# Optimization experiments

Measured on AMD Instinct MI355X. Metric: run time of the kernel, lower is better.

The kernel has to match this reference:

```python
import jax, jax.numpy as jnp
import numpy as np
import math

D_INNER = 512
D_STATE = 16
DT_RANK = 32
B_SZ = 2
L_SEQ = 4096


def setup_inputs() -> dict:
    key = jax.random.key(0)
    ks = jax.random.split(key, 6)
    x = jax.random.normal(ks[0], (B_SZ, L_SEQ, D_INNER), dtype=jnp.float32)
    # parameters (match torch init semantics closely enough for a numeric baseline)
    A = jnp.arange(1, D_STATE + 1, dtype=jnp.float32)
    A_log = jnp.broadcast_to(jnp.log(A)[None, :], (D_INNER, D_STATE)).copy()
    D_param = jnp.ones((D_INNER,), dtype=jnp.float32)
    # x_proj: Linear(d_inner -> dt_rank + 2*d_state), no bias
    W_xproj = jax.random.normal(ks[1], (DT_RANK + 2 * D_STATE, D_INNER), dtype=jnp.float32) / np.sqrt(D_INNER)
    # dt_proj: Linear(dt_rank -> d_inner) with special bias init
    W_dt = jax.random.normal(ks[2], (D_INNER, DT_RANK), dtype=jnp.float32) / np.sqrt(DT_RANK)
    dt_init = jnp.exp(jax.random.uniform(ks[3], (D_INNER,)) * (math.log(0.1) - math.log(0.001)) + math.log(0.001))
    b_dt = jnp.log(jnp.exp(dt_init) - 1.0)
    alpha = jnp.asarray(0.6, dtype=jnp.float32)
    beta_logit = jnp.asarray(math.log(0.99 / (1.0 - 0.99 + 1e-08)), dtype=jnp.float32)
    return {"x": x, "A_log": A_log, "D_param": D_param, "W_xproj": W_xproj,
            "W_dt": W_dt, "b_dt": b_dt, "alpha": alpha, "beta_logit": beta_logit}


def _momentum_ssm(x, A_log, D_param, W_xproj, W_dt, b_dt, alpha, beta_logit):
    # x: (B, L, D)
    proj = jnp.einsum('bld,pd->blp', x, W_xproj)            # (B, L, r+2N)
    dt_in = proj[..., :DT_RANK]
    Bp = proj[..., DT_RANK:DT_RANK + D_STATE]                # (B, L, N)
    Cp = proj[..., DT_RANK + D_STATE:]                       # (B, L, N)
    dt = jax.nn.softplus(jnp.einsum('blr,dr->bld', dt_in, W_dt) + b_dt)  # (B, L, D)
    A = -jnp.exp(A_log)                                      # (D, N)
    A_bar = jnp.exp(dt[..., None] * A[None, None])           # (B, L, D, N)
    # fused B_bar * x_t: dt * Bp * x
    inp = dt[..., None] * Bp[:, :, None, :] * x[..., None]   # (B, L, D, N)
    beta = jax.nn.sigmoid(beta_logit)

    # scan over time; carry (h, v): (B, D, N)
    h0 = jnp.zeros((x.shape[0], D_INNER, D_STATE), dtype=x.dtype)
    v0 = jnp.zeros_like(h0)

    def step(carry, ts):
        h, v = carry
        a_t, inp_t, c_t = ts                                 # (B,D,N), (B,D,N), (B,N)
        v = beta * v + alpha * inp_t
        h = a_t * h + v
        y = jnp.einsum('bdn,bn->bd', h, c_t)
        return (h, v), y

    xs = (jnp.moveaxis(A_bar, 1, 0), jnp.moveaxis(inp, 1, 0), jnp.moveaxis(Cp, 1, 0))
    _, ys = jax.lax.scan(step, (h0, v0), xs)                 # ys: (L, B, D)
    y = jnp.moveaxis(ys, 0, 1)                               # (B, L, D)
    return y + D_param * x


def reference(x, A_log, D_param, W_xproj, W_dt, b_dt, alpha, beta_logit):
    return _momentum_ssm(x, A_log, D_param, W_xproj, W_dt, b_dt, alpha, beta_logit)
```

## Files before the change

kernel.cpp:

```cpp
#include <hip/hip_runtime.h>


#define D_IN 512
#define D_ST 16
#define DTR  32
#define BSZ  2
#define LSEQ 4096
#define PDIM 64
#define NCH  128
#define LCH  (LSEQ / NCH)
#define LOG2E 1.44269504f

typedef __attribute__((ext_vector_type(8))) short short8;
typedef __attribute__((ext_vector_type(4))) float f32x4;

__device__ inline unsigned short bf16_rne(float f) {
  unsigned b = __float_as_uint(f);
  return (unsigned short)((b + 0x7fffu + ((b >> 16) & 1u)) >> 16);
}

__device__ inline void cvt8(const float4 u, const float4 v, short8& hi, short8& lo) {
  float f[8] = {u.x, u.y, u.z, u.w, v.x, v.y, v.z, v.w};
#pragma unroll
  for (int i = 0; i < 8; ++i) {
    unsigned short h = bf16_rne(f[i]);
    hi[i] = (short)h;
    float r = f[i] - __uint_as_float((unsigned)h << 16);
    lo[i] = (short)bf16_rne(r);
  }
}

__global__ __launch_bounds__(256) void k_wprep(const float* __restrict__ W,
                                               short* __restrict__ Whi,
                                               short* __restrict__ Wlo) {
  const int i = (blockIdx.x * 256 + threadIdx.x) * 4;
  float4 w = *(const float4*)(W + i);
  float f[4] = {w.x, w.y, w.z, w.w};
  unsigned short h[4], lo[4];
#pragma unroll
  for (int j = 0; j < 4; ++j) {
    h[j] = bf16_rne(f[j]);
    float r = f[j] - __uint_as_float((unsigned)h[j] << 16);
    lo[j] = bf16_rne(r);
  }
  *(uint2*)(Whi + i) = make_uint2(h[0] | ((unsigned)h[1] << 16), h[2] | ((unsigned)h[3] << 16));
  *(uint2*)(Wlo + i) = make_uint2(lo[0] | ((unsigned)lo[1] << 16), lo[2] | ((unsigned)lo[3] << 16));
}

#define MM3(ACC, AH, AL, BH, BL)                                        \
  ACC = __builtin_amdgcn_mfma_f32_16x16x32_bf16(AL, BH, ACC, 0, 0, 0);  \
  ACC = __builtin_amdgcn_mfma_f32_16x16x32_bf16(AH, BL, ACC, 0, 0, 0);  \
  ACC = __builtin_amdgcn_mfma_f32_16x16x32_bf16(AH, BH, ACC, 0, 0, 0);

#define LOADB(P, S)                                   \
  {                                                   \
    const int kb = ((S) & 15) * 32;                   \
    P##h0 = *(const short8*)(bh + kb);                \
    P##h1 = *(const short8*)(bh + 8192 + kb);         \
    P##h2 = *(const short8*)(bh + 16384 + kb);        \
    P##h3 = *(const short8*)(bh + 24576 + kb);        \
    P##l0 = *(const short8*)(bl + kb);                \
    P##l1 = *(const short8*)(bl + 8192 + kb);         \
    P##l2 = *(const short8*)(bl + 16384 + kb);        \
    P##l3 = *(const short8*)(bl + 24576 + kb);        \
  }

#define LOADA(Aa, Ab, S)                              \
  {                                                   \
    const int ka = ((S) & 15) * 32;                   \
    Aa = *(const float4*)(xr + ka);                   \
    Ab = *(const float4*)(xr + ka + 4);               \
  }

#define SUBSTEP(Aa, Ab, P, SA, SB)                    \
  {                                                   \
    short8 ahi, alo;                                  \
    cvt8(Aa, Ab, ahi, alo);                           \
    MM3(acc0, ahi, alo, P##h0, P##l0);                \
    MM3(acc1, ahi, alo, P##h1, P##l1);                \
    MM3(acc2, ahi, alo, P##h2, P##l2);                \
    MM3(acc3, ahi, alo, P##h3, P##l3);                \
    LOADB(P, SB);                                     \
    LOADA(Aa, Ab, SA);                                \
  }

__global__ __launch_bounds__(64) void k_proj(const float* __restrict__ x,
                                             const short* __restrict__ Whi,
                                             const short* __restrict__ Wlo,
                                             float* __restrict__ proj) {
  const int row0 = blockIdx.x * 16;
  const int l = threadIdx.x;
  const int m = l & 15;
  const int ko = (l >> 4) * 8;
  const float* xr = x + (size_t)(row0 + m) * D_IN + ko;
  const short* bh = Whi + (size_t)m * D_IN + ko;
  const short* bl = Wlo + (size_t)m * D_IN + ko;

  f32x4 acc0 = {0.f, 0.f, 0.f, 0.f}, acc1 = acc0, acc2 = acc0, acc3 = acc0;
  float4 A0a, A0b, A1a, A1b, A2a, A2b, A3a, A3b;
  short8 Xh0, Xh1, Xh2, Xh3, Xl0, Xl1, Xl2, Xl3;
  short8 Yh0, Yh1, Yh2, Yh3, Yl0, Yl1, Yl2, Yl3;
  LOADA(A0a, A0b, 0); LOADA(A1a, A1b, 1); LOADA(A2a, A2b, 2); LOADA(A3a, A3b, 3);
  LOADB(X, 0); LOADB(Y, 1);

#pragma unroll
  for (int it = 0; it < 4; ++it) {
    const int s = it * 4;
    SUBSTEP(A0a, A0b, X, s + 4, s + 2);
    SUBSTEP(A1a, A1b, Y, s + 5, s + 3);
    SUBSTEP(A2a, A2b, X, s + 6, s + 4);
    SUBSTEP(A3a, A3b, Y, s + 7, s + 5);
  }

  const int col = l & 15;
  const int r0 = (l >> 4) * 4;
#pragma unroll
  for (int r = 0; r < 4; ++r) {
    float* pr = proj + (size_t)(row0 + r0 + r) * PDIM + col;
    pr[0] = acc0[r]; pr[16] = acc1[r]; pr[32] = acc2[r]; pr[48] = acc3[r];
  }
}

__global__ __launch_bounds__(256) void k_dt(const float* __restrict__ proj,
                                            const float* __restrict__ W_dt,
                                            const float* __restrict__ b_dt,
                                            float* __restrict__ dt) {
  const int r0 = blockIdx.x * 8;
  const int d = blockIdx.y * 256 + threadIdx.x;
  float w[DTR];
  const float4* wp = (const float4*)(W_dt + (size_t)d * DTR);
#pragma unroll
  for (int i = 0; i < 8; ++i) ((float4*)w)[i] = wp[i];
  const float bb = b_dt[d];
#pragma unroll
  for (int r = 0; r < 8; ++r) {
    const float* pr = proj + (size_t)(r0 + r) * PDIM;
    float a0 = bb, a1 = 0.f, a2 = 0.f, a3 = 0.f;
#pragma unroll
    for (int k = 0; k < DTR; k += 4) {
      a0 = fmaf(pr[k + 0], w[k + 0], a0);
      a1 = fmaf(pr[k + 1], w[k + 1], a1);
      a2 = fmaf(pr[k + 2], w[k + 2], a2);
      a3 = fmaf(pr[k + 3], w[k + 3], a3);
    }
    float acc = (a0 + a1) + (a2 + a3);
    float sp = (acc > 20.f) ? acc : log1pf(__expf(acc));
    dt[(size_t)(r0 + r) * D_IN + d] = sp;
  }
}

#define S1_STEP(DC, XC, BC)                     \
  {                                             \
    sd += DC;                                   \
    bpow *= beta;                               \
    const float u = alpha * DC * XC;            \
    const float* Bf = (const float*)BC;         \
    _Pragma("unroll")                           \
    for (int n = 0; n < 16; ++n) {              \
      float a = exp2f(DC * A2[n]);              \
      v[n] = fmaf(beta, v[n], u * Bf[n]);       \
      h[n] = fmaf(a, h[n], v[n]);               \
      cv[n] = fmaf(a, cv[n], bpow);             \
    }                                           \
  }

__global__ __launch_bounds__(256) void k_scan1(const float* __restrict__ dt,
                                               const float* __restrict__ x,
                                               const float* __restrict__ proj,
                                               const float* __restrict__ A_log,
                                               const float* __restrict__ alpha_p,
                                               const float* __restrict__ beta_p,
                                               float* __restrict__ hh,
                                               float* __restrict__ vh,
                                               float* __restrict__ cvv,
                                               float* __restrict__ sdt) {
  const int c = blockIdx.x, b = blockIdx.z;
  const int d = blockIdx.y * 256 + threadIdx.x;
  const float alpha = alpha_p[0];
  const float beta = 1.f / (1.f + __expf(-beta_p[0]));
  float A2[D_ST];
  {
    const float4* ap = (const float4*)(A_log + (size_t)d * D_ST);
#pragma unroll
    for (int i = 0; i < 4; ++i) {
      float4 a4 = ap[i];
      A2[4 * i + 0] = -__expf(a4.x) * LOG2E;
      A2[4 * i + 1] = -__expf(a4.y) * LOG2E;
      A2[4 * i + 2] = -__expf(a4.z) * LOG2E;
      A2[4 * i + 3] = -__expf(a4.w) * LOG2E;
    }
  }
  float h[16] = {}, v[16] = {}, cv[16] = {};
  float bpow = 1.f, sd = 0.f;

  const int t0 = c * LCH;
  const float* dtp = dt + (size_t)b * LSEQ * D_IN + d;
  const float* xp = x + (size_t)b * LSEQ * D_IN + d;
  const float* bcp = proj + (size_t)b * LSEQ * PDIM + DTR;

  float d0 = dtp[(size_t)t0 * D_IN], x0v = xp[(size_t)t0 * D_IN];
  float d1 = dtp[(size_t)(t0 + 1) * D_IN], x1v = xp[(size_t)(t0 + 1) * D_IN];
  float4 B0[4], B1[4];
#pragma unroll
  for (int i = 0; i < 4; ++i) {
    B0[i] = *(const float4*)(bcp + (size_t)t0 * PDIM + 4 * i);
    B1[i] = *(const float4*)(bcp + (size_t)(t0 + 1) * PDIM + 4 * i);
  }

  for (int j = 0; j < LCH; j += 2) {
    const size_t ta = t0 + ((j + 2) & (LCH - 1));
    S1_STEP(d0, x0v, B0);
    d0 = dtp[ta * D_IN]; x0v = xp[ta * D_IN];
#pragma unroll
    for (int i = 0; i < 4; ++i) B0[i] = *(const float4*)(bcp + ta * PDIM + 4 * i);

    const size_t tb = t0 + ((j + 3) & (LCH - 1));
    S1_STEP(d1, x1v, B1);
    d1 = dtp[tb * D_IN]; x1v = xp[tb * D_IN];
#pragma unroll
    for (int i = 0; i < 4; ++i) B1[i] = *(const float4*)(bcp + tb * PDIM + 4 * i);
  }

  const size_t base = ((size_t)(b * NCH + c) * D_IN + d) * D_ST;
#pragma unroll
  for (int i = 0; i < 4; ++i) {
    *(float4*)(hh + base + 4 * i) = ((float4*)h)[i];
    *(float4*)(vh + base + 4 * i) = ((float4*)v)[i];
    *(float4*)(cvv + base + 4 * i) = ((float4*)cv)[i];
  }
  sdt[(size_t)(b * NCH + c) * D_IN + d] = sd;
}

__global__ __launch_bounds__(64) void k_fix(float* __restrict__ hh,
                                            float* __restrict__ vh,
                                            const float* __restrict__ cvv,
                                            const float* __restrict__ sdt,
                                            const float* __restrict__ A_log,
                                            const float* __restrict__ beta_p) {
  const int g = blockIdx.x * 64 + threadIdx.x;
  const int b = g >> 13;
  const int dn = g & 8191;
  const float beta = 1.f / (1.f + __expf(-beta_p[0]));
  const float A2 = -__expf(A_log[dn]) * LOG2E;
  float bL = beta;
#pragma unroll
  for (int i = 0; i < 5; ++i) bL *= bL;

  const size_t cs = (size_t)D_IN * D_ST;
  const size_t base = (size_t)b * NCH * cs + dn;
  const size_t sbase = (size_t)b * NCH * D_IN + (dn >> 4);

  float hg[4], vg[4], cg[4], sg[4];
#pragma unroll
  for (int i = 0; i < 4; ++i) {
    hg[i] = hh[base + i * cs];
    vg[i] = vh[base + i * cs];
    cg[i] = cvv[base + i * cs];
    sg[i] = sdt[sbase + i * D_IN];
  }
  float H = 0.f, V = 0.f;
  for (int c0 = 0; c0 < NCH; c0 += 4) {
    const int cp = (c0 + 4) & (NCH - 1);
    float hn[4], vn[4], cn[4], sn[4];
#pragma unroll
    for (int i = 0; i < 4; ++i) {
      hn[i] = hh[base + (size_t)(cp + i) * cs];
      vn[i] = vh[base + (size_t)(cp + i) * cs];
      cn[i] = cvv[base + (size_t)(cp + i) * cs];
      sn[i] = sdt[sbase + (size_t)(cp + i) * D_IN];
    }
#pragma unroll
    for (int i = 0; i < 4; ++i) {
      hh[base + (size_t)(c0 + i) * cs] = H;
      vh[base + (size_t)(c0 + i) * cs] = V;
      const float Pa = exp2f(sg[i] * A2);
      const float Hn = fmaf(Pa, H, fmaf(cg[i], V, hg[i]));
      V = fmaf(bL, V, vg[i]);
      H = Hn;
    }
#pragma unroll
    for (int i = 0; i < 4; ++i) { hg[i] = hn[i]; vg[i] = vn[i]; cg[i] = cn[i]; sg[i] = sn[i]; }
  }
}

#define S2_STEP(DC, XC, BC, TT)                                   \
  {                                                               \
    const float u = alpha * DC * XC;                              \
    const float* Bf = (const float*)BC;                           \
    float y0 = 0.f, y1 = 0.f, y2 = 0.f, y3 = 0.f;                 \
    _Pragma("unroll")                                             \
    for (int n = 0; n < 16; ++n) {                                \
      float a = exp2f(DC * A2[n]);                                \
      v[n] = fmaf(beta, v[n], u * Bf[n]);                         \
      h[n] = fmaf(a, h[n], v[n]);                                 \
      float hc = h[n] * Bf[16 + n];                               \
      if ((n & 3) == 0) y0 += hc;                                 \
      else if ((n & 3) == 1) y1 += hc;                            \
      else if ((n & 3) == 2) y2 += hc;                            \
      else y3 += hc;                                              \
    }                                                             \
    op[(size_t)(TT) * D_IN] = (y0 + y1) + (y2 + y3) + Dv * XC;    \
  }

__global__ __launch_bounds__(256) void k_scan2(const float* __restrict__ dt,
                                               const float* __restrict__ x,
                                               const float* __restrict__ proj,
                                               const float* __restrict__ A_log,
                                               const float* __restrict__ D_param,
                                               const float* __restrict__ alpha_p,
                                               const float* __restrict__ beta_p,
                                               const float* __restrict__ hh,
                                               const float* __restrict__ vh,
                                               float* __restrict__ out) {
  const int c = blockIdx.x, b = blockIdx.z;
  const int d = blockIdx.y * 256 + threadIdx.x;
  const float alpha = alpha_p[0];
  const float beta = 1.f / (1.f + __expf(-beta_p[0]));
  const float Dv = D_param[d];
  float A2[D_ST];
  {
    const float4* ap = (const float4*)(A_log + (size_t)d * D_ST);
#pragma unroll
    for (int i = 0; i < 4; ++i) {
      float4 a4 = ap[i];
      A2[4 * i + 0] = -__expf(a4.x) * LOG2E;
      A2[4 * i + 1] = -__expf(a4.y) * LOG2E;
      A2[4 * i + 2] = -__expf(a4.z) * LOG2E;
      A2[4 * i + 3] = -__expf(a4.w) * LOG2E;
    }
  }
  const size_t ibase = ((size_t)(b * NCH + c) * D_IN + d) * D_ST;
  float h[16], v[16];
#pragma unroll
  for (int i = 0; i < 4; ++i) {
    ((float4*)h)[i] = *(const float4*)(hh + ibase + 4 * i);
    ((float4*)v)[i] = *(const float4*)(vh + ibase + 4 * i);
  }

  const int t0 = c * LCH;
  const float* dtp = dt + (size_t)b * LSEQ * D_IN + d;
  const float* xp = x + (size_t)b * LSEQ * D_IN + d;
  const float* bcp = proj + (size_t)b * LSEQ * PDIM + DTR;
  float* op = out + (size_t)b * LSEQ * D_IN + d;

  float d0 = dtp[(size_t)t0 * D_IN], x0v = xp[(size_t)t0 * D_IN];
  float d1 = dtp[(size_t)(t0 + 1) * D_IN], x1v = xp[(size_t)(t0 + 1) * D_IN];
  float4 BC0[8], BC1[8];
#pragma unroll
  for (int i = 0; i < 8; ++i) {
    BC0[i] = *(const float4*)(bcp + (size_t)t0 * PDIM + 4 * i);
    BC1[i] = *(const float4*)(bcp + (size_t)(t0 + 1) * PDIM + 4 * i);
  }

  for (int j = 0; j < LCH; j += 2) {
    const size_t ta = t0 + ((j + 2) & (LCH - 1));
    S2_STEP(d0, x0v, BC0, t0 + j);
    d0 = dtp[ta * D_IN]; x0v = xp[ta * D_IN];
#pragma unroll
    for (int i = 0; i < 8; ++i) BC0[i] = *(const float4*)(bcp + ta * PDIM + 4 * i);

    const size_t tb = t0 + ((j + 3) & (LCH - 1));
    S2_STEP(d1, x1v, BC1, t0 + j + 1);
    d1 = dtp[tb * D_IN]; x1v = xp[tb * D_IN];
#pragma unroll
    for (int i = 0; i < 8; ++i) BC1[i] = *(const float4*)(bcp + tb * PDIM + 4 * i);
  }
}

extern "C" void kernel_launch(void* const* d_in, const int* in_sizes, int n_in,
                              void* d_out, int out_size, void* d_ws, size_t ws_size,
                              hipStream_t stream) {
  const float* x = (const float*)d_in[0];
  const float* A_log = (const float*)d_in[1];
  const float* D_param = (const float*)d_in[2];
  const float* W_xproj = (const float*)d_in[3];
  const float* W_dt = (const float*)d_in[4];
  const float* b_dt = (const float*)d_in[5];
  const float* alpha = (const float*)d_in[6];
  const float* beta_logit = (const float*)d_in[7];
  float* out = (float*)d_out;

  float* ws = (float*)d_ws;
  float* proj = ws;
  float* dt = proj + (size_t)BSZ * LSEQ * PDIM;
  float* hh = dt + (size_t)BSZ * LSEQ * D_IN;
  float* vh = hh + (size_t)BSZ * NCH * D_IN * D_ST;
  float* cvv = vh + (size_t)BSZ * NCH * D_IN * D_ST;
  float* sdt = cvv + (size_t)BSZ * NCH * D_IN * D_ST;
  short* Whi = (short*)(sdt + (size_t)BSZ * NCH * D_IN);
  short* Wlo = Whi + (size_t)PDIM * D_IN;

  k_wprep<<<dim3(PDIM * D_IN / 1024), dim3(256), 0, stream>>>(W_xproj, Whi, Wlo);
  k_proj<<<dim3(BSZ * LSEQ / 16), dim3(64), 0, stream>>>(x, Whi, Wlo, proj);
  k_dt<<<dim3(BSZ * LSEQ / 8, D_IN / 256), dim3(256), 0, stream>>>(proj, W_dt, b_dt, dt);
  k_scan1<<<dim3(NCH, D_IN / 256, BSZ), dim3(256), 0, stream>>>(
      dt, x, proj, A_log, alpha, beta_logit, hh, vh, cvv, sdt);
  k_fix<<<dim3(BSZ * D_IN * D_ST / 64), dim3(64), 0, stream>>>(hh, vh, cvv, sdt, A_log,
                                                               beta_logit);
  k_scan2<<<dim3(NCH, D_IN / 256, BSZ), dim3(256), 0, stream>>>(
      dt, x, proj, A_log, D_param, alpha, beta_logit, hh, vh, out);
}
```

Baseline: 194.4 us.

## Interleave dt and x, stage B/C in LDS, and preload chunk inputs in scans

k_dt now writes dt and x interleaved as float2, so the scans read one 8-byte stream instead of two separate arrays. Both scan kernels copy their chunk's B (and C) rows into shared memory once per block and bulk-load all 32 dt/x pairs into registers up front. This replaces the rolling two-step prefetch with a fully unrolled loop. k_fix widens its prefetch batch from 4 to 8 chunks. The cost is much higher register pressure (64 floats of dx plus state), which may reduce occupancy, plus an extra x copy written in k_dt.

```diff
diff --git a/kernel.cpp b/kernel.cpp
--- a/kernel.cpp
+++ b/kernel.cpp
@@ -124,7 +124,8 @@
 __global__ __launch_bounds__(256) void k_dt(const float* __restrict__ proj,
                                             const float* __restrict__ W_dt,
                                             const float* __restrict__ b_dt,
-                                            float* __restrict__ dt) {
+                                            const float* __restrict__ x,
+                                            float2* __restrict__ dtx) {
   const int r0 = blockIdx.x * 8;
   const int d = blockIdx.y * 256 + threadIdx.x;
   float w[DTR];
@@ -145,27 +146,12 @@
     }
     float acc = (a0 + a1) + (a2 + a3);
     float sp = (acc > 20.f) ? acc : log1pf(__expf(acc));
-    dt[(size_t)(r0 + r) * D_IN + d] = sp;
-  }
-}
-
-#define S1_STEP(DC, XC, BC)                     \
-  {                                             \
-    sd += DC;                                   \
-    bpow *= beta;                               \
-    const float u = alpha * DC * XC;            \
-    const float* Bf = (const float*)BC;         \
-    _Pragma("unroll")                           \
-    for (int n = 0; n < 16; ++n) {              \
-      float a = exp2f(DC * A2[n]);              \
-      v[n] = fmaf(beta, v[n], u * Bf[n]);       \
-      h[n] = fmaf(a, h[n], v[n]);               \
-      cv[n] = fmaf(a, cv[n], bpow);             \
-    }                                           \
-  }
-
-__global__ __launch_bounds__(256) void k_scan1(const float* __restrict__ dt,
-                                               const float* __restrict__ x,
+    float xv = x[(size_t)(r0 + r) * D_IN + d];
+    dtx[(size_t)(r0 + r) * D_IN + d] = make_float2(sp, xv);
+  }
+}
+
+__global__ __launch_bounds__(256) void k_scan1(const float2* __restrict__ dtx,
                                                const float* __restrict__ proj,
                                                const float* __restrict__ A_log,
                                                const float* __restrict__ alpha_p,
@@ -174,8 +160,18 @@
                                                float* __restrict__ vh,
                                                float* __restrict__ cvv,
                                                float* __restrict__ sdt) {
+  __shared__ float Bs[LCH][D_ST];
   const int c = blockIdx.x, b = blockIdx.z;
   const int d = blockIdx.y * 256 + threadIdx.x;
+  const int t0 = c * LCH;
+  {
+    const float* src = proj + ((size_t)b * LSEQ + t0) * PDIM + DTR;
+#pragma unroll
+    for (int k = 0; k < (LCH * D_ST) / 256; ++k) {
+      const int idx = threadIdx.x + k * 256;
+      Bs[idx >> 4][idx & 15] = src[(size_t)(idx >> 4) * PDIM + (idx & 15)];
+    }
+  }
   const float alpha = alpha_p[0];
   const float beta = 1.f / (1.f + __expf(-beta_p[0]));
   float A2[D_ST];
@@ -190,35 +186,31 @@
       A2[4 * i + 3] = -__expf(a4.w) * LOG2E;
     }
   }
+  float2 dx[LCH];
+  const float2* dp = dtx + (size_t)b * LSEQ * D_IN + d;
+#pragma unroll
+  for (int j = 0; j < LCH; ++j) dx[j] = dp[(size_t)(t0 + j) * D_IN];
+  __syncthreads();
+
   float h[16] = {}, v[16] = {}, cv[16] = {};
   float bpow = 1.f, sd = 0.f;
-
-  const int t0 = c * LCH;
-  const float* dtp = dt + (size_t)b * LSEQ * D_IN + d;
-  const float* xp = x + (size_t)b * LSEQ * D_IN + d;
-  const float* bcp = proj + (size_t)b * LSEQ * PDIM + DTR;
-
-  float d0 = dtp[(size_t)t0 * D_IN], x0v = xp[(size_t)t0 * D_IN];
-  float d1 = dtp[(size_t)(t0 + 1) * D_IN], x1v = xp[(size_t)(t0 + 1) * D_IN];
-  float4 B0[4], B1[4];
-#pragma unroll
-  for (int i = 0; i < 4; ++i) {
-    B0[i] = *(const float4*)(bcp + (size_t)t0 * PDIM + 4 * i);
-    B1[i] = *(const float4*)(bcp + (size_t)(t0 + 1) * PDIM + 4 * i);
-  }
-
-  for (int j = 0; j < LCH; j += 2) {
-    const size_t ta = t0 + ((j + 2) & (LCH - 1));
-    S1_STEP(d0, x0v, B0);
-    d0 = dtp[ta * D_IN]; x0v = xp[ta * D_IN];
-#pragma unroll
-    for (int i = 0; i < 4; ++i) B0[i] = *(const float4*)(bcp + ta * PDIM + 4 * i);
-
-    const size_t tb = t0 + ((j + 3) & (LCH - 1));
-    S1_STEP(d1, x1v, B1);
-    d1 = dtp[tb * D_IN]; x1v = xp[tb * D_IN];
-#pragma unroll
-    for (int i = 0; i < 4; ++i) B1[i] = *(const float4*)(bcp + tb * PDIM + 4 * i);
+#pragma unroll
+  for (int j = 0; j < LCH; ++j) {
+    const float dtv = dx[j].x, xv = dx[j].y;
+    sd += dtv;
+    bpow *= beta;
+    const float u = alpha * dtv * xv;
+    float4 Bq[4];
+#pragma unroll
+    for (int i = 0; i < 4; ++i) Bq[i] = ((const float4*)&Bs[j][0])[i];
+    const float* Bf = (const float*)Bq;
+#pragma unroll
+    for (int n = 0; n < 16; ++n) {
+      float a = exp2f(dtv * A2[n]);
+      v[n] = fmaf(beta, v[n], u * Bf[n]);
+      h[n] = fmaf(a, h[n], v[n]);
+      cv[n] = fmaf(a, cv[n], bpow);
+    }
   }
 
   const size_t base = ((size_t)(b * NCH + c) * D_IN + d) * D_ST;
@@ -250,27 +242,27 @@
   const size_t base = (size_t)b * NCH * cs + dn;
   const size_t sbase = (size_t)b * NCH * D_IN + (dn >> 4);
 
-  float hg[4], vg[4], cg[4], sg[4];
-#pragma unroll
-  for (int i = 0; i < 4; ++i) {
+  float hg[8], vg[8], cg[8], sg[8];
+#pragma unroll
+  for (int i = 0; i < 8; ++i) {
     hg[i] = hh[base + i * cs];
     vg[i] = vh[base + i * cs];
     cg[i] = cvv[base + i * cs];
     sg[i] = sdt[sbase + i * D_IN];
   }
   float H = 0.f, V = 0.f;
-  for (int c0 = 0; c0 < NCH; c0 += 4) {
-    const int cp = (c0 + 4) & (NCH - 1);
-    float hn[4], vn[4], cn[4], sn[4];
-#pragma unroll
-    for (int i = 0; i < 4; ++i) {
+  for (int c0 = 0; c0 < NCH; c0 += 8) {
+    const int cp = (c0 + 8) & (NCH - 1);
+    float hn[8], vn[8], cn[8], sn[8];
+#pragma unroll
+    for (int i = 0; i < 8; ++i) {
       hn[i] = hh[base + (size_t)(cp + i) * cs];
       vn[i] = vh[base + (size_t)(cp + i) * cs];
       cn[i] = cvv[base + (size_t)(cp + i) * cs];
       sn[i] = sdt[sbase + (size_t)(cp + i) * D_IN];
     }
 #pragma unroll
-    for (int i = 0; i < 4; ++i) {
+    for (int i = 0; i < 8; ++i) {
       hh[base + (size_t)(c0 + i) * cs] = H;
       vh[base + (size_t)(c0 + i) * cs] = V;
       const float Pa = exp2f(sg[i] * A2);
@@ -279,31 +271,11 @@
       H = Hn;
     }
 #pragma unroll
-    for (int i = 0; i < 4; ++i) { hg[i] = hn[i]; vg[i] = vn[i]; cg[i] = cn[i]; sg[i] = sn[i]; }
-  }
-}
-
-#define S2_STEP(DC, XC, BC, TT)                                   \
-  {                                                               \
-    const float u = alpha * DC * XC;                              \
-    const float* Bf = (const float*)BC;                           \
-    float y0 = 0.f, y1 = 0.f, y2 = 0.f, y3 = 0.f;                 \
-    _Pragma("unroll")                                             \
-    for (int n = 0; n < 16; ++n) {                                \
-      float a = exp2f(DC * A2[n]);                                \
-      v[n] = fmaf(beta, v[n], u * Bf[n]);                         \
-      h[n] = fmaf(a, h[n], v[n]);                                 \
-      float hc = h[n] * Bf[16 + n];                               \
-      if ((n & 3) == 0) y0 += hc;                                 \
-      else if ((n & 3) == 1) y1 += hc;                            \
-      else if ((n & 3) == 2) y2 += hc;                            \
-      else y3 += hc;                                              \
-    }                                                             \
-    op[(size_t)(TT) * D_IN] = (y0 + y1) + (y2 + y3) + Dv * XC;    \
-  }
-
-__global__ __launch_bounds__(256) void k_scan2(const float* __restrict__ dt,
-                                               const float* __restrict__ x,
+    for (int i = 0; i < 8; ++i) { hg[i] = hn[i]; vg[i] = vn[i]; cg[i] = cn[i]; sg[i] = sn[i]; }
+  }
+}
+
+__global__ __launch_bounds__(256) void k_scan2(const float2* __restrict__ dtx,
                                                const float* __restrict__ proj,
                                                const float* __restrict__ A_log,
                                                const float* __restrict__ D_param,
@@ -312,8 +284,18 @@
                                                const float* __restrict__ hh,
                                                const float* __restrict__ vh,
                                                float* __restrict__ out) {
+  __shared__ float BCs[LCH][2 * D_ST];
   const int c = blockIdx.x, b = blockIdx.z;
   const int d = blockIdx.y * 256 + threadIdx.x;
+  const int t0 = c * LCH;
+  {
+    const float* src = proj + ((size_t)b * LSEQ + t0) * PDIM + DTR;
+#pragma unroll
+    for (int k = 0; k < (LCH * 2 * D_ST) / 256; ++k) {
+      const int idx = threadIdx.x + k * 256;
+      BCs[idx >> 5][idx & 31] = src[(size_t)(idx >> 5) * PDIM + (idx & 31)];
+    }
+  }
   const float alpha = alpha_p[0];
   const float beta = 1.f / (1.f + __expf(-beta_p[0]));
   const float Dv = D_param[d];
@@ -336,34 +318,34 @@
     ((float4*)h)[i] = *(const float4*)(hh + ibase + 4 * i);
     ((float4*)v)[i] = *(const float4*)(vh + ibase + 4 * i);
   }
-
-  const int t0 = c * LCH;
-  const float* dtp = dt + (size_t)b * LSEQ * D_IN + d;
-  const float* xp = x + (size_t)b * LSEQ * D_IN + d;
-  const float* bcp = proj + (size_t)b * LSEQ * PDIM + DTR;
+  float2 dx[LCH];
+  const float2* dp = dtx + (size_t)b * LSEQ * D_IN + d;
+#pragma unroll
+  for (int j = 0; j < LCH; ++j) dx[j] = dp[(size_t)(t0 + j) * D_IN];
+  __syncthreads();
+
   float* op = out + (size_t)b * LSEQ * D_IN + d;
-
-  float d0 = dtp[(size_t)t0 * D_IN], x0v = xp[(size_t)t0 * D_IN];
-  float d1 = dtp[(size_t)(t0 + 1) * D_IN], x1v = xp[(size_t)(t0 + 1) * D_IN];
-  float4 BC0[8], BC1[8];
-#pragma unroll
-  for (int i = 0; i < 8; ++i) {
-    BC0[i] = *(const float4*)(bcp + (size_t)t0 * PDIM + 4 * i);
-    BC1[i] = *(const float4*)(bcp + (size_t)(t0 + 1) * PDIM + 4 * i);
-  }
-
-  for (int j = 0; j < LCH; j += 2) {
-    const size_t ta = t0 + ((j + 2) & (LCH - 1));
-    S2_STEP(d0, x0v, BC0, t0 + j);
-    d0 = dtp[ta * D_IN]; x0v = xp[ta * D_IN];
-#pragma unroll
-    for (int i = 0; i < 8; ++i) BC0[i] = *(const float4*)(bcp + ta * PDIM + 4 * i);
-
-    const size_t tb = t0 + ((j + 3) & (LCH - 1));
-    S2_STEP(d1, x1v, BC1, t0 + j + 1);
-    d1 = dtp[tb * D_IN]; x1v = xp[tb * D_IN];
-#pragma unroll
-    for (int i = 0; i < 8; ++i) BC1[i] = *(const float4*)(bcp + tb * PDIM + 4 * i);
+#pragma unroll
+  for (int j = 0; j < LCH; ++j) {
+    const float dtv = dx[j].x, xv = dx[j].y;
+    const float u = alpha * dtv * xv;
+    float4 Bq[8];
+#pragma unroll
+    for (int i = 0; i < 8; ++i) Bq[i] = ((const float4*)&BCs[j][0])[i];
+    const float* Bf = (const float*)Bq;
+    float y0 = 0.f, y1 = 0.f, y2 = 0.f, y3 = 0.f;
+#pragma unroll
+    for (int n = 0; n < 16; ++n) {
+      float a = exp2f(dtv * A2[n]);
+      v[n] = fmaf(beta, v[n], u * Bf[n]);
+      h[n] = fmaf(a, h[n], v[n]);
+      float hc = h[n] * Bf[16 + n];
+      if ((n & 3) == 0) y0 += hc;
+      else if ((n & 3) == 1) y1 += hc;
+      else if ((n & 3) == 2) y2 += hc;
+      else y3 += hc;
+    }
+    op[(size_t)(t0 + j) * D_IN] = (y0 + y1) + (y2 + y3) + Dv * xv;
   }
 }
 
@@ -382,8 +364,8 @@
 
   float* ws = (float*)d_ws;
   float* proj = ws;
-  float* dt = proj + (size_t)BSZ * LSEQ * PDIM;
-  float* hh = dt + (size_t)BSZ * LSEQ * D_IN;
+  float2* dtx = (float2*)(proj + (size_t)BSZ * LSEQ * PDIM);
+  float* hh = (float*)(dtx + (size_t)BSZ * LSEQ * D_IN);
   float* vh = hh + (size_t)BSZ * NCH * D_IN * D_ST;
   float* cvv = vh + (size_t)BSZ * NCH * D_IN * D_ST;
   float* sdt = cvv + (size_t)BSZ * NCH * D_IN * D_ST;
@@ -392,11 +374,11 @@
 
   k_wprep<<<dim3(PDIM * D_IN / 1024), dim3(256), 0, stream>>>(W_xproj, Whi, Wlo);
   k_proj<<<dim3(BSZ * LSEQ / 16), dim3(64), 0, stream>>>(x, Whi, Wlo, proj);
-  k_dt<<<dim3(BSZ * LSEQ / 8, D_IN / 256), dim3(256), 0, stream>>>(proj, W_dt, b_dt, dt);
+  k_dt<<<dim3(BSZ * LSEQ / 8, D_IN / 256), dim3(256), 0, stream>>>(proj, W_dt, b_dt, x, dtx);
   k_scan1<<<dim3(NCH, D_IN / 256, BSZ), dim3(256), 0, stream>>>(
-      dt, x, proj, A_log, alpha, beta_logit, hh, vh, cvv, sdt);
+      dtx, proj, A_log, alpha, beta_logit, hh, vh, cvv, sdt);
   k_fix<<<dim3(BSZ * D_IN * D_ST / 64), dim3(64), 0, stream>>>(hh, vh, cvv, sdt, A_log,
                                                                beta_logit);
   k_scan2<<<dim3(NCH, D_IN / 256, BSZ), dim3(256), 0, stream>>>(
-      dt, x, proj, A_log, D_param, alpha, beta_logit, hh, vh, out);
-}
+      dtx, proj, A_log, D_param, alpha, beta_logit, hh, vh, out);
+}
```

Measured after the change: 199.7 us. 2.7% more time.
